# Optimization experiments

Hardware: AMD Instinct MI355X
Metric: run time of the kernel (lower is better)

## Reference

```python
import jax, jax.numpy as jnp
import numpy as np
from jax import lax

B, H, W, C, NH = 16, 56, 56, 192, 6
L = H * W
DH = C // NH            # 32
HID = 4 * C             # 768
ETA = 1.0 / DH          # TTT inner-loop learning rate
EPS = 1e-5

# ---- RoPE rotation tables (deterministic buffer, shape (H, W, C//2)) ----
_kmax = C // 4
_theta = 1.0 / (10000.0 ** (np.arange(_kmax) / _kmax))
_ii, _jj = np.meshgrid(np.arange(H), np.arange(W), indexing='ij')
_ang = np.concatenate([_ii[..., None] * _theta, _jj[..., None] * _theta], axis=-1)  # (H,W,C/2)
_COS = jnp.asarray(np.cos(_ang), dtype=jnp.float32)
_SIN = jnp.asarray(np.sin(_ang), dtype=jnp.float32)


def layernorm(x, g, b):
    mu = jnp.mean(x, axis=-1, keepdims=True)
    var = jnp.mean(jnp.square(x - mu), axis=-1, keepdims=True)
    return (x - mu) * lax.rsqrt(var + EPS) * g + b


def dwconv3x3(x_blc, w, b):
    # x: (B, L, Ch) -> depthwise 3x3 conv over (H, W) -> (B, L, Ch)
    Ch = x_blc.shape[-1]
    xi = x_blc.reshape(B, H, W, Ch).transpose(0, 3, 1, 2)  # NCHW
    y = lax.conv_general_dilated(xi, w, (1, 1), 'SAME', feature_group_count=Ch,
                                 dimension_numbers=('NCHW', 'OIHW', 'NCHW'))
    y = y + b[None, :, None, None]
    return y.transpose(0, 2, 3, 1).reshape(B, L, Ch)


def rope(x):
    # x: (B, L, C); rotate complex pairs with 2D axial angles
    xr = x.reshape(B, H, W, C // 2, 2)
    re, im = xr[..., 0], xr[..., 1]
    o_re = _COS * re - _SIN * im
    o_im = _SIN * re + _COS * im
    return jnp.stack([o_re, o_im], axis=-1).reshape(B, L, C)


def ttt_attn(xn, qkv_w, qkv_b, W0, proj_w, proj_b):
    qkv = xn @ qkv_w.T + qkv_b                      # (B, L, 3C)
    q, k, v = jnp.split(qkv, 3, axis=-1)
    q = rope(q) * (DH ** -0.5)
    k = rope(k)

    def to_heads(t):  # (B,L,C) -> (L, B*NH, DH)
        return t.reshape(B, L, NH, DH).transpose(1, 0, 2, 3).reshape(L, B * NH, DH)
    qs, ks, vs = to_heads(q), to_heads(k), to_heads(v)

    Wst0 = jnp.broadcast_to(W0[None], (B, NH, DH, DH)).reshape(B * NH, DH, DH)

    def step(Wst, qkv_t):
        qt, kt, vt = qkv_t
        pred = jnp.einsum('bij,bj->bi', Wst, kt)
        Wn = Wst - ETA * (pred - vt)[:, :, None] * kt[:, None, :]
        ot = jnp.einsum('bij,bj->bi', Wn, qt)
        return Wn, ot

    _, out = lax.scan(step, Wst0, (qs, ks, vs))     # out: (L, B*NH, DH)
    out = out.reshape(L, B, NH, DH).transpose(1, 0, 2, 3).reshape(B, L, C)
    return out @ proj_w.T + proj_b


def setup_inputs() -> dict:
    key = jax.random.key(0)
    ks = jax.random.split(key, 12)
    s = 0.02
    return {
        'x': jax.random.normal(ks[0], (B, L, C), jnp.float32),
        'cpe_w': jax.random.normal(ks[1], (C, 1, 3, 3), jnp.float32) * s,
        'cpe_b': jnp.zeros((C,), jnp.float32),
        'n1_g': jnp.ones((C,), jnp.float32),
        'n1_b': jnp.zeros((C,), jnp.float32),
        'qkv_w': jax.random.normal(ks[2], (3 * C, C), jnp.float32) * s,
        'qkv_b': jnp.zeros((3 * C,), jnp.float32),
        'W0': jax.random.normal(ks[3], (NH, DH, DH), jnp.float32) * s,
        'proj_w': jax.random.normal(ks[4], (C, C), jnp.float32) * s,
        'proj_b': jnp.zeros((C,), jnp.float32),
        'n2_g': jnp.ones((C,), jnp.float32),
        'n2_b': jnp.zeros((C,), jnp.float32),
        'fc1_w': jax.random.normal(ks[5], (HID, C), jnp.float32) * s,
        'fc1_b': jnp.zeros((HID,), jnp.float32),
        'dwc_w': jax.random.normal(ks[6], (HID, 1, 3, 3), jnp.float32) * s,
        'dwc_b': jnp.zeros((HID,), jnp.float32),
        'fc2_w': jax.random.normal(ks[7], (C, HID), jnp.float32) * s,
        'fc2_b': jnp.zeros((C,), jnp.float32),
    }


def reference(x, cpe_w, cpe_b, n1_g, n1_b, qkv_w, qkv_b, W0, proj_w, proj_b,
              n2_g, n2_b, fc1_w, fc1_b, dwc_w, dwc_b, fc2_w, fc2_b):
    # CPE: conditional positional encoding (depthwise conv residual)
    x = x + dwconv3x3(x, cpe_w, cpe_b)
    # TTT attention branch
    x = x + ttt_attn(layernorm(x, n1_g, n1_b), qkv_w, qkv_b, W0, proj_w, proj_b)
    # MLP branch with depthwise conv
    h1 = jax.nn.gelu(layernorm(x, n2_g, n2_b) @ fc1_w.T + fc1_b, approximate=False)
    h1 = jax.nn.gelu(h1 + dwconv3x3(h1, dwc_w, dwc_b), approximate=False)
    x = x + (h1 @ fc2_w.T + fc2_b)
    return x
```

## Files before the change

kernel.cpp:

```cpp
#include <hip/hip_runtime.h>
#include <hip/hip_bf16.h>

#define Bc 16
#define Hc 56
#define Wcc 56
#define Cc 192
#define NHc 6
#define Lc 3136
#define DHc 32
#define HIDc 768
#define NHEAD 96
#define Sc 32
#define NCHUNK 98
#define NPAIR (NHEAD*NCHUNK)
#define ROWS (Bc*Lc)
#define GROUPROWS (ROWS/4)
#define ETAc (1.0f/32.0f)

typedef unsigned short u16;
typedef unsigned int u32;
typedef __attribute__((ext_vector_type(8))) short bf16x8;
typedef __attribute__((ext_vector_type(4))) float f32x4;
typedef __attribute__((ext_vector_type(16))) float f32x16;

__device__ __forceinline__ float b2f(u16 v){ u32 u = ((u32)v)<<16; float f; __builtin_memcpy(&f,&u,4); return f; }
__device__ __forceinline__ u16 f2b(float f){ u32 u; __builtin_memcpy(&u,&f,4); u32 r = u + 0x7FFFu + ((u>>16)&1u); return (u16)(r>>16); }
__device__ __forceinline__ f32x16 zero16(){ f32x16 z = {0,0,0,0,0,0,0,0,0,0,0,0,0,0,0,0}; return z; }

__device__ __forceinline__ void make_bfrags(const f32x16& t, int hi, bf16x8& b1, bf16x8& b2){
  u32 P[8], S[8];
  #pragma unroll
  for (int q=0;q<4;q++){
    #pragma unroll
    for (int j=0;j<2;j++){
      u32 r; float lo = t[4*q+2*j], hv = t[4*q+2*j+1];
      asm("v_cvt_pk_bf16_f32 %0, %1, %2" : "=v"(r) : "v"(lo), "v"(hv));
      P[2*q+j] = r;
    }
  }
  #pragma unroll
  for (int i=0;i<8;i++) S[i] = (u32)__shfl_xor((int)P[i], 32);
  union { u32 u[4]; bf16x8 v; } f1, f2;
  if (hi==0){ f1.u[0]=P[0]; f1.u[1]=P[1]; f1.u[2]=S[0]; f1.u[3]=S[1];
              f2.u[0]=P[4]; f2.u[1]=P[5]; f2.u[2]=S[4]; f2.u[3]=S[5]; }
  else      { f1.u[0]=S[2]; f1.u[1]=S[3]; f1.u[2]=P[2]; f1.u[3]=P[3];
              f2.u[0]=S[6]; f2.u[1]=S[7]; f2.u[2]=P[6]; f2.u[3]=P[7]; }
  b1 = f1.v; b2 = f2.v;
}

__global__ __launch_bounds__(256) void cast_bf16_kernel(const float* __restrict__ src, u16* __restrict__ dst, int n){
  int i = blockIdx.x*256 + threadIdx.x;
  if (i < n) dst[i] = f2b(src[i]);
}

__global__ __launch_bounds__(256) void dwt_kernel(const float* __restrict__ w, float* __restrict__ wt, int CH){
  int i = blockIdx.x*256 + threadIdx.x;
  if (i < CH*9){ int ch = i/9, t = i - ch*9; wt[t*CH + ch] = w[i]; }
}

__global__ __launch_bounds__(256) void rope_tab_kernel(float* __restrict__ ct, float* __restrict__ st){
  int i = blockIdx.x*256 + threadIdx.x;
  int l = i/96, p = i - l*96;
  int h = l/Wcc, w = l - h*Wcc;
  int kk = (p<48)? p : p-48;
  float th = powf(10000.f, -(float)kk/48.f);
  float ang = (float)((p<48)? h : w) * th;
  ct[i] = cosf(ang);
  st[i] = sinf(ang);
}

__global__ __launch_bounds__(256) void cpe_kernel(const float* __restrict__ x, const float* __restrict__ cwt9,
                                                  const float* __restrict__ bs, u16* __restrict__ x1){
  int gid = blockIdx.x*256 + threadIdx.x;
  int cg = gid % 24; int row = gid / 24; int ch0 = cg*8;
  int l = row % Lc; int h = l/Wcc, w = l - h*Wcc;
  const float* xp = x + (size_t)row*Cc + ch0;
  float acc[8];
  { f32x4 b0 = *(const f32x4*)(bs+ch0), b1v = *(const f32x4*)(bs+ch0+4);
    acc[0]=b0[0];acc[1]=b0[1];acc[2]=b0[2];acc[3]=b0[3];
    acc[4]=b1v[0];acc[5]=b1v[1];acc[6]=b1v[2];acc[7]=b1v[3]; }
  #pragma unroll
  for (int kh=0;kh<3;kh++){
    int hh = h+kh-1; if (hh<0 || hh>=Hc) continue;
    #pragma unroll
    for (int kw=0;kw<3;kw++){
      int ww = w+kw-1; if (ww<0 || ww>=Wcc) continue;
      const float* ip = xp + ((kh-1)*Wcc + (kw-1))*Cc;
      f32x4 i0 = *(const f32x4*)ip, i1 = *(const f32x4*)(ip+4);
      const float* wp = cwt9 + (kh*3+kw)*Cc + ch0;
      f32x4 w0 = *(const f32x4*)wp, w1 = *(const f32x4*)(wp+4);
      acc[0] += i0[0]*w0[0]; acc[1] += i0[1]*w0[1]; acc[2] += i0[2]*w0[2]; acc[3] += i0[3]*w0[3];
      acc[4] += i1[0]*w1[0]; acc[5] += i1[1]*w1[1]; acc[6] += i1[2]*w1[2]; acc[7] += i1[3]*w1[3];
    }
  }
  f32x4 c0 = *(const f32x4*)xp, c1 = *(const f32x4*)(xp+4);
  union { bf16x8 v; u16 s[8]; } ov;
  ov.s[0]=f2b(c0[0]+acc[0]); ov.s[1]=f2b(c0[1]+acc[1]); ov.s[2]=f2b(c0[2]+acc[2]); ov.s[3]=f2b(c0[3]+acc[3]);
  ov.s[4]=f2b(c1[0]+acc[4]); ov.s[5]=f2b(c1[1]+acc[5]); ov.s[6]=f2b(c1[2]+acc[6]); ov.s[7]=f2b(c1[3]+acc[7]);
  *(bf16x8*)(x1 + (size_t)row*Cc + ch0) = ov.v;
}

template<int INF32>
__global__ __launch_bounds__(256) void ln_kernel(const u16* __restrict__ xb, const float* __restrict__ xf,
                                                 const float* __restrict__ g, const float* __restrict__ b,
                                                 u16* __restrict__ out){
  int row = blockIdx.x*4 + (threadIdx.x>>6);
  int lane = threadIdx.x & 63;
  float v0, v1, v2;
  if (INF32){
    const float* xr = xf + (size_t)row*Cc;
    v0 = xr[lane]; v1 = xr[lane+64]; v2 = xr[lane+128];
  } else {
    const u16* xr = xb + (size_t)row*Cc;
    v0 = b2f(xr[lane]); v1 = b2f(xr[lane+64]); v2 = b2f(xr[lane+128]);
  }
  float s = v0+v1+v2;
  float q = v0*v0 + v1*v1 + v2*v2;
  #pragma unroll
  for (int off=32; off; off>>=1){ s += __shfl_xor(s, off); q += __shfl_xor(q, off); }
  float mu = s*(1.f/Cc);
  float var = q*(1.f/Cc) - mu*mu;
  float rs = rsqrtf(var + 1e-5f);
  u16* orow = out + (size_t)row*Cc;
  orow[lane]     = f2b((v0-mu)*rs*g[lane]     + b[lane]);
  orow[lane+64]  = f2b((v1-mu)*rs*g[lane+64]  + b[lane+64]);
  orow[lane+128] = f2b((v2-mu)*rs*g[lane+128] + b[lane+128]);
}

template<int MODE>
__global__ __launch_bounds__(256) void gemm_kernel(
    const u16* __restrict__ A, const u16* __restrict__ Wt,
    const float* __restrict__ bias, int K,
    float* __restrict__ outf, u16* __restrict__ outb,
    u16* __restrict__ vdst, const u16* __restrict__ residb, const float* __restrict__ residf)
{
  int wid = threadIdx.x>>6, lane = threadIdx.x&63;
  int m0 = blockIdx.x*64 + (wid>>1)*32;
  int n0 = blockIdx.y*192 + (wid&1)*96;
  int ar = lane&15, kg = (lane>>4)*8;
  f32x4 acc[2][6];
  #pragma unroll
  for (int r=0;r<2;r++)
    #pragma unroll
    for (int c=0;c<6;c++){ f32x4 z = {0.f,0.f,0.f,0.f}; acc[r][c] = z; }
  for (int k0=0;k0<K;k0+=32){
    bf16x8 af[2], bfr[6];
    #pragma unroll
    for (int r=0;r<2;r++) af[r] = *(const bf16x8*)(A + (size_t)(m0 + r*16 + ar)*K + k0 + kg);
    #pragma unroll
    for (int c=0;c<6;c++) bfr[c] = *(const bf16x8*)(Wt + (size_t)(n0 + c*16 + ar)*K + k0 + kg);
    #pragma unroll
    for (int r=0;r<2;r++)
      #pragma unroll
      for (int c=0;c<6;c++)
        acc[r][c] = __builtin_amdgcn_mfma_f32_16x16x32_bf16(af[r], bfr[c], acc[r][c], 0,0,0);
  }
  int rb = (lane>>4)*4;
  #pragma unroll
  for (int r=0;r<2;r++){
    #pragma unroll
    for (int c=0;c<6;c++){
      int col = n0 + c*16 + ar;
      float bv = bias[col];
      #pragma unroll
      for (int j=0;j<4;j++){
        int row = m0 + r*16 + rb + j;
        float v = acc[r][c][j] + bv;
        if (MODE==0){
          if (col < 384) outb[(size_t)row*384 + col] = f2b(v);
          else {
            int bb = row/Lc; int l = row - bb*Lc;
            int nh = (col-384)>>5; int d = col&31;
            vdst[(((size_t)(bb*NHc+nh))*Lc + l)*DHc + d] = f2b(v);
          }
        } else if (MODE==1){
          outf[(size_t)row*Cc + col] = v + b2f(residb[(size_t)row*Cc + col]);
        } else if (MODE==2){
          float gv = 0.5f*v*(1.f + erff(v*0.70710678118654752f));
          outb[(size_t)row*HIDc + col] = f2b(gv);
        } else {
          outf[(size_t)row*Cc + col] = v + residf[(size_t)row*Cc + col];
        }
      }
    }
  }
}

__global__ __launch_bounds__(256) void rope_kernel(const u16* __restrict__ qk, const float* __restrict__ ct,
                                                   const float* __restrict__ st, u16* __restrict__ q_s, u16* __restrict__ k_s){
  int gid = blockIdx.x*256 + threadIdx.x;
  int sub = gid % 24; int row = gid / 24;
  int bb = row / Lc; int l = row - bb*Lc;
  bool isq = sub < 12; int pg = isq ? sub : sub-12;
  int p0 = pg*8;
  int cbase = (isq ? 0 : 192) + 2*p0;
  const u16* qr = qk + (size_t)row*384 + cbase;
  bf16x8 in0 = *(const bf16x8*)qr;
  bf16x8 in1 = *(const bf16x8*)(qr + 8);
  const float* cp = ct + l*96 + p0;
  const float* sp = st + l*96 + p0;
  f32x4 c0 = *(const f32x4*)cp, c1 = *(const f32x4*)(cp+4);
  f32x4 s0 = *(const f32x4*)sp, s1 = *(const f32x4*)(sp+4);
  float cs[8] = {c0[0],c0[1],c0[2],c0[3],c1[0],c1[1],c1[2],c1[3]};
  float sn[8] = {s0[0],s0[1],s0[2],s0[3],s1[0],s1[1],s1[2],s1[3]};
  float sc = isq ? 0.1767766952966369f : 1.0f;
  union { bf16x8 v; u16 s[8]; } o0, o1;
  #pragma unroll
  for (int j=0;j<4;j++){
    float re = b2f((u16)in0[2*j]), im = b2f((u16)in0[2*j+1]);
    o0.s[2*j]   = f2b((cs[j]*re - sn[j]*im)*sc);
    o0.s[2*j+1] = f2b((sn[j]*re + cs[j]*im)*sc);
  }
  #pragma unroll
  for (int j=0;j<4;j++){
    float re = b2f((u16)in1[2*j]), im = b2f((u16)in1[2*j+1]);
    o1.s[2*j]   = f2b((cs[4+j]*re - sn[4+j]*im)*sc);
    o1.s[2*j+1] = f2b((sn[4+j]*re + cs[4+j]*im)*sc);
  }
  int nh = pg>>1, d0 = (pg&1)*16;
  u16* dst = (isq ? q_s : k_s) + (((size_t)(bb*NHc+nh))*Lc + l)*DHc + d0;
  *(bf16x8*)dst = o0.v;
  *(bf16x8*)(dst+8) = o1.v;
}

__global__ __launch_bounds__(64) void ttta_kernel(const u16* __restrict__ k_s, const u16* __restrict__ v_s,
                                                  u16* __restrict__ u_s, u16* __restrict__ rn_s,
                                                  u16* __restrict__ af_s, u16* __restrict__ bc_s){
  __shared__ float Gl[1024];
  __shared__ u16 LK[32*40];
  __shared__ float LU[32*33];
  __shared__ float LR[32*33];
  int pair = blockIdx.x;
  int head = pair / NCHUNK;
  int l0 = (pair - head*NCHUNK) * Sc;
  int lane = threadIdx.x; int rr = lane&31; int hi = lane>>5; int ks = hi*8;
  const u16* kb = k_s + ((size_t)head*Lc + l0)*DHc;
  bf16x8 a0 = *(const bf16x8*)(kb + rr*32 + ks);
  bf16x8 a1 = *(const bf16x8*)(kb + rr*32 + 16 + ks);
  *(bf16x8*)(LK + rr*40 + ks) = a0;
  *(bf16x8*)(LK + rr*40 + 16 + ks) = a1;
  f32x16 g = zero16();
  g = __builtin_amdgcn_mfma_f32_32x32x16_bf16(a0, a0, g, 0,0,0);
  g = __builtin_amdgcn_mfma_f32_32x32x16_bf16(a1, a1, g, 0,0,0);
  #pragma unroll
  for (int reg=0;reg<16;reg++){
    int i = (reg&3) + 8*(reg>>2) + 4*hi;
    Gl[i*32 + rr] = ETAc * g[reg];
  }
  __syncthreads();
  float X[32];
  if (lane < 32){
    #pragma unroll
    for (int i=0;i<32;i++) X[i] = ETAc * b2f(v_s[((size_t)head*Lc + l0 + i)*DHc + lane]);
  } else {
    int m = lane-32;
    #pragma unroll
    for (int i=0;i<32;i++) X[i] = ETAc * b2f(kb[i*32 + m]);
  }
  #pragma unroll
  for (int i=1;i<32;i++){
    float a = X[i];
    #pragma unroll
    for (int j=0;j<i;j++) a -= Gl[i*32+j]*X[j];
    X[i] = a;
  }
  if (lane < 32){
    u16* dst = u_s + (size_t)pair*1024 + lane;
    #pragma unroll
    for (int i=0;i<32;i++) dst[i*32] = f2b(X[i]);
    #pragma unroll
    for (int i=0;i<32;i++) LU[lane*33 + i] = X[i];
  } else {
    u16* dst = rn_s + (size_t)pair*1024 + (lane&31);
    #pragma unroll
    for (int i=0;i<32;i++) dst[i*32] = f2b(-X[i]);
    #pragma unroll
    for (int i=0;i<32;i++) LR[(lane&31)*33 + i] = X[i];
  }
  __syncthreads();
  union { bf16x8 v; u16 s[8]; } kc1, kc2, uc1, uc2, rc1, rc2;
  #pragma unroll
  for (int s=0;s<8;s++){
    kc1.s[s] = LK[(ks+s)*40 + rr];
    kc2.s[s] = LK[(16+ks+s)*40 + rr];
    uc1.s[s] = f2b(LU[rr*33 + ks+s]);
    uc2.s[s] = f2b(LU[rr*33 + 16+ks+s]);
    rc1.s[s] = f2b(LR[rr*33 + ks+s]);
    rc2.s[s] = f2b(LR[rr*33 + 16+ks+s]);
  }
  f32x16 bacc = zero16();
  bacc = __builtin_amdgcn_mfma_f32_32x32x16_bf16(kc1.v, uc1.v, bacc, 0,0,0);
  bacc = __builtin_amdgcn_mfma_f32_32x32x16_bf16(kc2.v, uc2.v, bacc, 0,0,0);
  union { bf16x8 v; u16 s[8]; } bo1, bo2;
  #pragma unroll
  for (int r=0;r<8;r++){ bo1.s[r] = f2b(bacc[r]); bo2.s[r] = f2b(bacc[8+r]); }
  *(bf16x8*)(bc_s + (size_t)pair*1024 + lane*16) = bo1.v;
  *(bf16x8*)(bc_s + (size_t)pair*1024 + lane*16 + 8) = bo2.v;
  f32x16 aacc = zero16();
  aacc = __builtin_amdgcn_mfma_f32_32x32x16_bf16(rc1.v, kc1.v, aacc, 0,0,0);
  aacc = __builtin_amdgcn_mfma_f32_32x32x16_bf16(rc2.v, kc2.v, aacc, 0,0,0);
  f32x16 an;
  #pragma unroll
  for (int r=0;r<16;r++) an[r] = -aacc[r];
  bf16x8 f1, f2;
  make_bfrags(an, hi, f1, f2);
  *(bf16x8*)(af_s + (size_t)pair*1024 + lane*16) = f1;
  *(bf16x8*)(af_s + (size_t)pair*1024 + lane*16 + 8) = f2;
}

__global__ __launch_bounds__(64) void tttb_kernel(const u16* __restrict__ af_s, const u16* __restrict__ bc_s,
                                                  const float* __restrict__ W0, u16* __restrict__ w_snap){
  int head = blockIdx.x; int nh = head % NHc;
  int lane = threadIdx.x; int rr = lane&31; int hi = lane>>5;
  f32x16 T;
  const float* w0r = W0 + nh*1024 + rr*32 + 4*hi;
  #pragma unroll
  for (int q=0;q<4;q++){
    f32x4 v = *(const f32x4*)(w0r + 8*q);
    T[4*q+0]=v[0]; T[4*q+1]=v[1]; T[4*q+2]=v[2]; T[4*q+3]=v[3];
  }
  size_t hb = (size_t)head*NCHUNK;
  const bf16x8* afp = (const bf16x8*)(af_s + hb*1024);
  const bf16x8* bcp = (const bf16x8*)(bc_s + hb*1024);
  bf16x8 A1 = afp[lane*2], A2 = afp[lane*2+1];
  bf16x8 Bv1 = bcp[lane*2], Bv2 = bcp[lane*2+1];
  bf16x8 b1, b2;
  make_bfrags(T, hi, b1, b2);
  for (int c=0;c<NCHUNK;c++){
    bf16x8 nA1=A1, nA2=A2, nB1=Bv1, nB2=Bv2;
    if (c+1 < NCHUNK){
      int base = (c+1)*128 + lane*2;
      nA1 = afp[base]; nA2 = afp[base+1];
      nB1 = bcp[base]; nB2 = bcp[base+1];
    }
    u16* wrow = w_snap + (hb + c)*1024 + rr*32;
    *(bf16x8*)(wrow + hi*8) = b1;
    *(bf16x8*)(wrow + 16 + hi*8) = b2;
    f32x16 acc;
    #pragma unroll
    for (int r=0;r<8;r++){ acc[r] = T[r] + b2f((u16)Bv1[r]); acc[8+r] = T[8+r] + b2f((u16)Bv2[r]); }
    acc = __builtin_amdgcn_mfma_f32_32x32x16_bf16(A1, b1, acc, 0,0,0);
    acc = __builtin_amdgcn_mfma_f32_32x32x16_bf16(A2, b2, acc, 0,0,0);
    T = acc;
    make_bfrags(T, hi, b1, b2);
    A1=nA1; A2=nA2; Bv1=nB1; Bv2=nB2;
  }
}

__global__ __launch_bounds__(64) void tttc_kernel(const u16* __restrict__ q_s, const u16* __restrict__ k_s,
                                                  const u16* __restrict__ w_snap, const u16* __restrict__ u_s,
                                                  const u16* __restrict__ rn_s, u16* __restrict__ o_bf){
  __shared__ __align__(16) u16 Pl[32*40];
  int pair = blockIdx.x;
  int head = pair / NCHUNK;
  int ch = pair - head*NCHUNK;
  int l0 = ch*Sc;
  int lane = threadIdx.x; int rr = lane&31; int hi = lane>>5; int ks = hi*8;
  const u16* qb = q_s + ((size_t)head*Lc + l0)*DHc;
  const u16* kb = k_s + ((size_t)head*Lc + l0)*DHc;
  bf16x8 q0 = *(const bf16x8*)(qb + rr*32 + ks);
  bf16x8 q1 = *(const bf16x8*)(qb + rr*32 + 16 + ks);
  bf16x8 k0 = *(const bf16x8*)(kb + rr*32 + ks);
  bf16x8 k1 = *(const bf16x8*)(kb + rr*32 + 16 + ks);
  f32x16 p = zero16();
  p = __builtin_amdgcn_mfma_f32_32x32x16_bf16(q0, k0, p, 0,0,0);
  p = __builtin_amdgcn_mfma_f32_32x32x16_bf16(q1, k1, p, 0,0,0);
  #pragma unroll
  for (int reg=0;reg<16;reg++){
    int i = (reg&3)+8*(reg>>2)+4*hi;
    Pl[i*40+rr] = (rr<=i) ? f2b(p[reg]) : (u16)0;
  }
  const u16* wsb = w_snap + (size_t)pair*1024;
  bf16x8 tb0 = *(const bf16x8*)(wsb + rr*32 + ks);
  bf16x8 tb1 = *(const bf16x8*)(wsb + rr*32 + 16 + ks);
  const u16* ub = u_s + (size_t)pair*1024;
  f32x16 wr;
  #pragma unroll
  for (int r=0;r<16;r++){
    int i = (r&3)+8*(r>>2)+4*hi;
    wr[r] = b2f(ub[i*32 + rr]);
  }
  const u16* rb = rn_s + (size_t)pair*1024;
  bf16x8 rn0 = *(const bf16x8*)(rb + rr*32 + ks);
  bf16x8 rn1 = *(const bf16x8*)(rb + rr*32 + 16 + ks);
  wr = __builtin_amdgcn_mfma_f32_32x32x16_bf16(rn0, tb0, wr, 0,0,0);
  wr = __builtin_amdgcn_mfma_f32_32x32x16_bf16(rn1, tb1, wr, 0,0,0);
  bf16x8 wb0, wb1;
  make_bfrags(wr, hi, wb0, wb1);
  __syncthreads();
  f32x16 o = zero16();
  o = __builtin_amdgcn_mfma_f32_32x32x16_bf16(q0, tb0, o, 0,0,0);
  o = __builtin_amdgcn_mfma_f32_32x32x16_bf16(q1, tb1, o, 0,0,0);
  bf16x8 pa0 = *(const bf16x8*)(Pl + rr*40 + ks);
  bf16x8 pa1 = *(const bf16x8*)(Pl + rr*40 + 16 + ks);
  o = __builtin_amdgcn_mfma_f32_32x32x16_bf16(pa0, wb0, o, 0,0,0);
  o = __builtin_amdgcn_mfma_f32_32x32x16_bf16(pa1, wb1, o, 0,0,0);
  int bb = head/NHc, nh = head - bb*NHc;
  #pragma unroll
  for (int reg=0;reg<16;reg++){
    int i = (reg&3)+8*(reg>>2)+4*hi;
    o_bf[((size_t)(bb*Lc + l0 + i))*Cc + nh*32 + rr] = f2b(o[reg]);
  }
}

__global__ __launch_bounds__(256) void dwc_kernel(const u16* __restrict__ h1, const float* __restrict__ wt9,
                                                  const float* __restrict__ bs, u16* __restrict__ h2, int row0){
  int gid = blockIdx.x*256 + threadIdx.x;
  int cg = gid % 96; int lrow = gid / 96; int ch0 = cg*8;
  int row = row0 + lrow;
  int l = row % Lc; int h = l/Wcc, w = l - h*Wcc;
  const u16* hp = h1 + (size_t)lrow*HIDc + ch0;
  float acc[8];
  { f32x4 b0 = *(const f32x4*)(bs+ch0), b1v = *(const f32x4*)(bs+ch0+4);
    acc[0]=b0[0];acc[1]=b0[1];acc[2]=b0[2];acc[3]=b0[3];
    acc[4]=b1v[0];acc[5]=b1v[1];acc[6]=b1v[2];acc[7]=b1v[3]; }
  #pragma unroll
  for (int kh=0;kh<3;kh++){
    int hh = h+kh-1; if (hh<0 || hh>=Hc) continue;
    #pragma unroll
    for (int kw=0;kw<3;kw++){
      int ww = w+kw-1; if (ww<0 || ww>=Wcc) continue;
      bf16x8 iv = *(const bf16x8*)(hp + ((kh-1)*Wcc + (kw-1))*HIDc);
      const float* wp = wt9 + (kh*3+kw)*HIDc + ch0;
      f32x4 w0 = *(const f32x4*)wp, w1 = *(const f32x4*)(wp+4);
      acc[0] += b2f((u16)iv[0])*w0[0]; acc[1] += b2f((u16)iv[1])*w0[1];
      acc[2] += b2f((u16)iv[2])*w0[2]; acc[3] += b2f((u16)iv[3])*w0[3];
      acc[4] += b2f((u16)iv[4])*w1[0]; acc[5] += b2f((u16)iv[5])*w1[1];
      acc[6] += b2f((u16)iv[6])*w1[2]; acc[7] += b2f((u16)iv[7])*w1[3];
    }
  }
  bf16x8 cv = *(const bf16x8*)hp;
  union { bf16x8 v; u16 s[8]; } ov;
  #pragma unroll
  for (int j=0;j<8;j++){
    float v = b2f((u16)cv[j]) + acc[j];
    ov.s[j] = f2b(0.5f*v*(1.f + erff(v*0.70710678118654752f)));
  }
  *(bf16x8*)(h2 + (size_t)lrow*HIDc + ch0) = ov.v;
}

extern "C" void kernel_launch(void* const* d_in, const int* in_sizes, int n_in,
                              void* d_out, int out_size, void* d_ws, size_t ws_size,
                              hipStream_t stream){
  const float* x     = (const float*)d_in[0];
  const float* cpe_w = (const float*)d_in[1];
  const float* cpe_b = (const float*)d_in[2];
  const float* n1_g  = (const float*)d_in[3];
  const float* n1_b  = (const float*)d_in[4];
  const float* qkv_w = (const float*)d_in[5];
  const float* qkv_b = (const float*)d_in[6];
  const float* W0    = (const float*)d_in[7];
  const float* proj_w= (const float*)d_in[8];
  const float* proj_b= (const float*)d_in[9];
  const float* n2_g  = (const float*)d_in[10];
  const float* n2_b  = (const float*)d_in[11];
  const float* fc1_w = (const float*)d_in[12];
  const float* fc1_b = (const float*)d_in[13];
  const float* dwc_w = (const float*)d_in[14];
  const float* dwc_b = (const float*)d_in[15];
  const float* fc2_w = (const float*)d_in[16];
  const float* fc2_b = (const float*)d_in[17];

  char* ws = (char*)d_ws;
  size_t off = 0;
  auto alloc = [&](size_t bytes)->char*{
    char* p = ws + off;
    off += (bytes + 255) & ~(size_t)255;
    return p;
  };
  u16* wbqkv = (u16*)alloc((size_t)576*192*2);
  u16* wbproj= (u16*)alloc((size_t)192*192*2);
  u16* wbfc1 = (u16*)alloc((size_t)768*192*2);
  u16* wbfc2 = (u16*)alloc((size_t)192*768*2);
  float* dwt9 = (float*)alloc((size_t)9*HIDc*4);
  float* cwt9 = (float*)alloc((size_t)9*Cc*4);
  float* ctab = (float*)alloc((size_t)Lc*96*4);
  float* stab = (float*)alloc((size_t)Lc*96*4);
  u16* regA = (u16*)alloc((size_t)ROWS*Cc*2);
  u16* regB = (u16*)alloc((size_t)ROWS*Cc*2);
  u16* regD = (u16*)alloc((size_t)NHEAD*Lc*DHc*2);
  u16* regE = (u16*)alloc((size_t)NHEAD*Lc*DHc*2);
  u16* rn_s = (u16*)alloc((size_t)NPAIR*1024*2);
  u16* af_s = (u16*)alloc((size_t)NPAIR*1024*2);
  u16* wsn  = (u16*)alloc((size_t)NPAIR*1024*2);
  u16* qk = (u16*)d_out;
  u16* us = (u16*)d_out;
  u16* bc = us + (size_t)NPAIR*1024;
  float* x2 = (float*)d_out;

  u16* x1 = regA;
  u16* xn = regB;
  u16* qs = regB;
  u16* xn2 = regB;
  u16* vs = regD;
  u16* obf = regD;
  u16* ksb = regE;

  cast_bf16_kernel<<<(576*192+255)/256,256,0,stream>>>(qkv_w, wbqkv, 576*192);
  cast_bf16_kernel<<<(192*192+255)/256,256,0,stream>>>(proj_w, wbproj, 192*192);
  cast_bf16_kernel<<<(768*192+255)/256,256,0,stream>>>(fc1_w, wbfc1, 768*192);
  cast_bf16_kernel<<<(192*768+255)/256,256,0,stream>>>(fc2_w, wbfc2, 192*768);
  dwt_kernel<<<(768*9+255)/256,256,0,stream>>>(dwc_w, dwt9, HIDc);
  dwt_kernel<<<(192*9+255)/256,256,0,stream>>>(cpe_w, cwt9, Cc);
  rope_tab_kernel<<<(Lc*96)/256,256,0,stream>>>(ctab, stab);

  cpe_kernel<<<(ROWS*24)/256,256,0,stream>>>(x, cwt9, cpe_b, x1);
  ln_kernel<0><<<ROWS/4,256,0,stream>>>(x1, nullptr, n1_g, n1_b, xn);
  { dim3 g(ROWS/64, 3); gemm_kernel<0><<<g,256,0,stream>>>(xn, wbqkv, qkv_b, 192, nullptr, qk, vs, nullptr, nullptr); }
  rope_kernel<<<(ROWS*24)/256,256,0,stream>>>(qk, ctab, stab, qs, ksb);
  ttta_kernel<<<NPAIR,64,0,stream>>>(ksb, vs, us, rn_s, af_s, bc);
  tttb_kernel<<<NHEAD,64,0,stream>>>(af_s, bc, W0, wsn);
  tttc_kernel<<<NPAIR,64,0,stream>>>(qs, ksb, wsn, us, rn_s, obf);
  { dim3 g(ROWS/64, 1); gemm_kernel<1><<<g,256,0,stream>>>(obf, wbproj, proj_b, 192, x2, nullptr, nullptr, x1, nullptr); }
  ln_kernel<1><<<ROWS/4,256,0,stream>>>(nullptr, x2, n2_g, n2_b, xn2);
  for (int g4=0; g4<4; g4++){
    const u16* a_in = xn2 + (size_t)g4*GROUPROWS*Cc;
    u16* h1 = regA;
    u16* h2 = regD;
    float* xo = x2 + (size_t)g4*GROUPROWS*Cc;
    { dim3 g(GROUPROWS/64, 4); gemm_kernel<2><<<g,256,0,stream>>>(a_in, wbfc1, fc1_b, 192, nullptr, h1, nullptr, nullptr, nullptr); }
    dwc_kernel<<<(GROUPROWS*96)/256,256,0,stream>>>(h1, dwt9, dwc_b, h2, g4*GROUPROWS);
    { dim3 g(GROUPROWS/64, 1); gemm_kernel<3><<<g,256,0,stream>>>(h2, wbfc2, fc2_b, 768, xo, nullptr, nullptr, nullptr, xo); }
  }
}
```

Measured before the change: 597.1 us.

## Stage GEMM A-tiles in LDS, prefetch weight fragments, halve MLP row groups

New measurement: 553.6 us. 7.3% less time.

```diff
diff --git a/kernel.cpp b/kernel.cpp
--- a/kernel.cpp
+++ b/kernel.cpp
@@ -14,7 +14,7 @@
 #define NCHUNK 98
 #define NPAIR (NHEAD*NCHUNK)
 #define ROWS (Bc*Lc)
-#define GROUPROWS (ROWS/4)
+#define GR2 (ROWS/2)
 #define ETAc (1.0f/32.0f)
 
 typedef unsigned short u16;
@@ -127,45 +127,75 @@
   orow[lane+128] = f2b((v2-mu)*rs*g[lane+128] + b[lane+128]);
 }
 
-template<int MODE>
+template<int MODE, int BLKM, int KT>
 __global__ __launch_bounds__(256) void gemm_kernel(
     const u16* __restrict__ A, const u16* __restrict__ Wt,
-    const float* __restrict__ bias, int K,
+    const float* __restrict__ bias,
     float* __restrict__ outf, u16* __restrict__ outb,
     u16* __restrict__ vdst, const u16* __restrict__ residb, const float* __restrict__ residf)
 {
-  int wid = threadIdx.x>>6, lane = threadIdx.x&63;
-  int m0 = blockIdx.x*64 + (wid>>1)*32;
-  int n0 = blockIdx.y*192 + (wid&1)*96;
-  int ar = lane&15, kg = (lane>>4)*8;
-  f32x4 acc[2][6];
-  #pragma unroll
-  for (int r=0;r<2;r++)
-    #pragma unroll
-    for (int c=0;c<6;c++){ f32x4 z = {0.f,0.f,0.f,0.f}; acc[r][c] = z; }
-  for (int k0=0;k0<K;k0+=32){
-    bf16x8 af[2], bfr[6];
-    #pragma unroll
-    for (int r=0;r<2;r++) af[r] = *(const bf16x8*)(A + (size_t)(m0 + r*16 + ar)*K + k0 + kg);
-    #pragma unroll
-    for (int c=0;c<6;c++) bfr[c] = *(const bf16x8*)(Wt + (size_t)(n0 + c*16 + ar)*K + k0 + kg);
-    #pragma unroll
-    for (int r=0;r<2;r++)
+  constexpr int WROWS = BLKM/2;
+  constexpr int NF = WROWS/16;
+  constexpr int NCH = KT/192;
+  constexpr int NG = BLKM*192/(256*8);
+  __shared__ u16 As[BLKM*200];
+  int tid = threadIdx.x;
+  int wid = tid>>6, lane = tid&63;
+  int wr = wid>>1, wc = wid&1;
+  int m0 = blockIdx.x*BLKM;
+  int n0 = blockIdx.y*192 + wc*96;
+  int ar = lane&15, kg = lane>>4;
+  f32x4 acc[NF][6];
+  #pragma unroll
+  for (int f=0;f<NF;f++)
+    #pragma unroll
+    for (int c=0;c<6;c++){ f32x4 z = {0.f,0.f,0.f,0.f}; acc[f][c] = z; }
+  bf16x8 bcur[6], bnxt[6];
+  #pragma unroll
+  for (int c=0;c<6;c++) bcur[c] = *(const bf16x8*)(Wt + (size_t)(n0 + c*16 + ar)*KT + kg*8);
+  #pragma unroll
+  for (int ch=0; ch<NCH; ch++){
+    if (ch>0) __syncthreads();
+    #pragma unroll
+    for (int j=0;j<NG;j++){
+      int g = j*256 + tid;
+      int grow = g/24, gcol = (g - grow*24)*8;
+      bf16x8 v = *(const bf16x8*)(A + (size_t)(m0+grow)*KT + ch*192 + gcol);
+      *(bf16x8*)(As + grow*200 + gcol) = v;
+    }
+    __syncthreads();
+    #pragma unroll
+    for (int kc=0;kc<6;kc++){
+      int s = ch*6 + kc;
+      if (s+1 < NCH*6){
+        int koff = ((s+1)/6)*192 + ((s+1)%6)*32 + kg*8;
+        #pragma unroll
+        for (int c=0;c<6;c++) bnxt[c] = *(const bf16x8*)(Wt + (size_t)(n0 + c*16 + ar)*KT + koff);
+      }
+      bf16x8 af[NF];
       #pragma unroll
-      for (int c=0;c<6;c++)
-        acc[r][c] = __builtin_amdgcn_mfma_f32_16x16x32_bf16(af[r], bfr[c], acc[r][c], 0,0,0);
-  }
-  int rb = (lane>>4)*4;
-  #pragma unroll
-  for (int r=0;r<2;r++){
+      for (int f=0;f<NF;f++)
+        af[f] = *(const bf16x8*)(As + (wr*WROWS + f*16 + ar)*200 + kc*32 + kg*8);
+      #pragma unroll
+      for (int f=0;f<NF;f++)
+        #pragma unroll
+        for (int c=0;c<6;c++)
+          acc[f][c] = __builtin_amdgcn_mfma_f32_16x16x32_bf16(af[f], bcur[c], acc[f][c], 0,0,0);
+      #pragma unroll
+      for (int c=0;c<6;c++) bcur[c] = bnxt[c];
+    }
+  }
+  int rb = kg*4;
+  #pragma unroll
+  for (int f=0;f<NF;f++){
     #pragma unroll
     for (int c=0;c<6;c++){
       int col = n0 + c*16 + ar;
       float bv = bias[col];
       #pragma unroll
       for (int j=0;j<4;j++){
-        int row = m0 + r*16 + rb + j;
-        float v = acc[r][c][j] + bv;
+        int row = m0 + wr*WROWS + f*16 + rb + j;
+        float v = acc[f][c][j] + bv;
         if (MODE==0){
           if (col < 384) outb[(size_t)row*384 + col] = f2b(v);
           else {
@@ -495,6 +525,8 @@
   u16* vs = regD;
   u16* obf = regD;
   u16* ksb = regE;
+  u16* h1 = regD;
+  u16* h2 = rn_s;
 
   cast_bf16_kernel<<<(576*192+255)/256,256,0,stream>>>(qkv_w, wbqkv, 576*192);
   cast_bf16_kernel<<<(192*192+255)/256,256,0,stream>>>(proj_w, wbproj, 192*192);
@@ -506,20 +538,18 @@
 
   cpe_kernel<<<(ROWS*24)/256,256,0,stream>>>(x, cwt9, cpe_b, x1);
   ln_kernel<0><<<ROWS/4,256,0,stream>>>(x1, nullptr, n1_g, n1_b, xn);
-  { dim3 g(ROWS/64, 3); gemm_kernel<0><<<g,256,0,stream>>>(xn, wbqkv, qkv_b, 192, nullptr, qk, vs, nullptr, nullptr); }
+  { dim3 g(ROWS/128, 3); gemm_kernel<0,128,192><<<g,256,0,stream>>>(xn, wbqkv, qkv_b, nullptr, qk, vs, nullptr, nullptr); }
   rope_kernel<<<(ROWS*24)/256,256,0,stream>>>(qk, ctab, stab, qs, ksb);
   ttta_kernel<<<NPAIR,64,0,stream>>>(ksb, vs, us, rn_s, af_s, bc);
   tttb_kernel<<<NHEAD,64,0,stream>>>(af_s, bc, W0, wsn);
   tttc_kernel<<<NPAIR,64,0,stream>>>(qs, ksb, wsn, us, rn_s, obf);
-  { dim3 g(ROWS/64, 1); gemm_kernel<1><<<g,256,0,stream>>>(obf, wbproj, proj_b, 192, x2, nullptr, nullptr, x1, nullptr); }
+  { dim3 g(ROWS/128, 1); gemm_kernel<1,128,192><<<g,256,0,stream>>>(obf, wbproj, proj_b, x2, nullptr, nullptr, x1, nullptr); }
   ln_kernel<1><<<ROWS/4,256,0,stream>>>(nullptr, x2, n2_g, n2_b, xn2);
-  for (int g4=0; g4<4; g4++){
-    const u16* a_in = xn2 + (size_t)g4*GROUPROWS*Cc;
-    u16* h1 = regA;
-    u16* h2 = regD;
-    float* xo = x2 + (size_t)g4*GROUPROWS*Cc;
-    { dim3 g(GROUPROWS/64, 4); gemm_kernel<2><<<g,256,0,stream>>>(a_in, wbfc1, fc1_b, 192, nullptr, h1, nullptr, nullptr, nullptr); }
-    dwc_kernel<<<(GROUPROWS*96)/256,256,0,stream>>>(h1, dwt9, dwc_b, h2, g4*GROUPROWS);
-    { dim3 g(GROUPROWS/64, 1); gemm_kernel<3><<<g,256,0,stream>>>(h2, wbfc2, fc2_b, 768, xo, nullptr, nullptr, nullptr, xo); }
-  }
-}
+  for (int g4=0; g4<2; g4++){
+    const u16* a_in = xn2 + (size_t)g4*GR2*Cc;
+    float* xo = x2 + (size_t)g4*GR2*Cc;
+    { dim3 g(GR2/128, 4); gemm_kernel<2,128,192><<<g,256,0,stream>>>(a_in, wbfc1, fc1_b, nullptr, h1, nullptr, nullptr, nullptr); }
+    dwc_kernel<<<(GR2*96)/256,256,0,stream>>>(h1, dwt9, dwc_b, h2, g4*GR2);
+    { dim3 g(GR2/64, 1); gemm_kernel<3,64,768><<<g,256,0,stream>>>(h2, wbfc2, fc2_b, xo, nullptr, nullptr, nullptr, xo); }
+  }
+}
```
